# Performance work log

Hardware: AMD Instinct MI355X
Metric: run time of the kernel (lower is better)

Reference implementation:

```python
import jax, jax.numpy as jnp
import numpy as np

# Body-part joint index groups (NTU-25 layout), as in the torch module
TORSO = np.array([0, 1, 2, 3, 20])
LEFT_HAND = np.array([8, 9, 10, 11, 23, 24])
LEFT_LEG = np.array([16, 17, 18, 19])
RIGHT_HAND = np.array([4, 5, 6, 7, 21, 22])
RIGHT_LEG = np.array([12, 13, 14, 15])
GROUPS = [TORSO, LEFT_HAND, LEFT_LEG, RIGHT_HAND, RIGHT_LEG]

N, C, T, V = 64, 256, 64, 25
HID = C // 16


def setup_inputs() -> dict:
    key = jax.random.key(0)
    k = jax.random.split(key, 5)
    x = jax.random.normal(k[0], (N, C, T, V), dtype=jnp.float32)
    # 5 branch MLPs (1x1 convs == linear over channels), stacked on leading axis f
    W1s = jax.random.normal(k[1], (5, HID, C), dtype=jnp.float32) * (1.0 / np.sqrt(C))
    b1s = jax.random.normal(k[2], (5, HID), dtype=jnp.float32) * 0.01
    W2s = jax.random.normal(k[3], (5, C, HID), dtype=jnp.float32) * (1.0 / np.sqrt(HID))
    b2s = jax.random.normal(k[4], (5, C), dtype=jnp.float32) * 0.01
    return {"x": x, "W1s": W1s, "b1s": b1s, "W2s": W2s, "b2s": b2s}


def _branch_mlp(p, W1s, b1s, W2s, b2s):
    # p: [N, C] pooled features; apply all 5 branch MLPs at once -> [N, 5, C]
    h = jax.nn.relu(jnp.einsum("nc,fhc->nfh", p, W1s) + b1s[None])  # [N,5,HID]
    return jnp.einsum("nfh,fch->nfc", h, W2s) + b2s[None]  # [N,5,C]


def reference(x, W1s, b1s, W2s, b2s):
    torso = x[:, :, :, TORSO]  # [N,C,T,5]
    avg = jnp.mean(torso, axis=(2, 3))  # [N,C] (AdaptiveAvgPool2d(1))
    mx = jnp.max(torso, axis=(2, 3))  # [N,C] (AdaptiveMaxPool2d(1))
    gates = jax.nn.sigmoid(_branch_mlp(avg, W1s, b1s, W2s, b2s)
                           + _branch_mlp(mx, W1s, b1s, W2s, b2s))  # [N,5,C]
    parts = [x[:, :, :, idx] * gates[:, i][:, :, None, None]
             for i, idx in enumerate(GROUPS)]
    return jnp.concatenate(parts, axis=3)  # [N,C,T,25]
```

## Files before the change

### kernel.cpp

```cpp
#include <hip/hip_runtime.h>
#include <math.h>

#define NB   64
#define CC   256
#define TT   64
#define VV   25
#define HID  16
#define NG   5
#define ROWF 1600
#define ROWF4 400
#define PAIRS 4

#define TORSO_MASK 0x10000Fu

__constant__ int PERM_LUT[25] = {
    0|(0<<8), 1|(0<<8), 2|(0<<8), 3|(0<<8), 20|(0<<8),
    8|(1<<8), 9|(1<<8), 10|(1<<8), 11|(1<<8), 23|(1<<8), 24|(1<<8),
    16|(2<<8), 17|(2<<8), 18|(2<<8), 19|(2<<8),
    4|(3<<8), 5|(3<<8), 6|(3<<8), 7|(3<<8), 21|(3<<8), 22|(3<<8),
    12|(4<<8), 13|(4<<8), 14|(4<<8), 15|(4<<8)
};

__global__ void pool_kernel(const float4* __restrict__ x4,
                            float* __restrict__ avg_out,
                            float* __restrict__ max_out) {
    const int wave = threadIdx.x >> 6;
    const int lane = threadIdx.x & 63;
    const int pair = blockIdx.x * 4 + wave;
    const int base4 = pair * ROWF4;

    float s = 0.0f;
    float m = -3.4e38f;
    for (int i = lane; i < ROWF4; i += 64) {
        float4 v = x4[base4 + i];
        const int e = 4 * i;
        int j = e % 25;
        float vals[4] = {v.x, v.y, v.z, v.w};
        #pragma unroll
        for (int k = 0; k < 4; ++k) {
            int jj = j + k;
            if (jj >= 25) jj -= 25;
            if ((TORSO_MASK >> jj) & 1u) {
                s += vals[k];
                m = fmaxf(m, vals[k]);
            }
        }
    }
    #pragma unroll
    for (int off = 32; off >= 1; off >>= 1) {
        s += __shfl_xor(s, off, 64);
        m = fmaxf(m, __shfl_xor(m, off, 64));
    }
    if (lane == 0) {
        avg_out[pair] = s * (1.0f / (TT * 5));
        max_out[pair] = m;
    }
}

__global__ void gates_kernel(const float* __restrict__ avg_in,
                             const float* __restrict__ max_in,
                             const float* __restrict__ W1s,
                             const float* __restrict__ b1s,
                             const float* __restrict__ W2s,
                             const float* __restrict__ b2s,
                             float* __restrict__ gates) {
    __shared__ float4 sAvg[CC / 4];
    __shared__ float4 sMax[CC / 4];
    __shared__ float sHA[NG * HID];
    __shared__ float sHM[NG * HID];

    const int n = blockIdx.x;
    const int tid = threadIdx.x;

    if (tid < 64)       sAvg[tid]      = reinterpret_cast<const float4*>(avg_in + n * CC)[tid];
    else if (tid < 128) sMax[tid - 64] = reinterpret_cast<const float4*>(max_in + n * CC)[tid - 64];
    __syncthreads();

    if (tid < 2 * NG * HID) {
        const int type = tid / (NG * HID);
        const int rem  = tid % (NG * HID);
        const float4* p = type ? sMax : sAvg;
        const float4* w = reinterpret_cast<const float4*>(W1s + rem * CC);
        float h = b1s[rem];
        #pragma unroll 8
        for (int c4 = 0; c4 < CC / 4; ++c4) {
            float4 a = w[c4], b = p[c4];
            h += a.x * b.x + a.y * b.y + a.z * b.z + a.w * b.w;
        }
        h = fmaxf(h, 0.0f);
        if (type) sHM[rem] = h; else sHA[rem] = h;
    }
    __syncthreads();

    const int c = tid;
    #pragma unroll
    for (int f = 0; f < NG; ++f) {
        const float4* w2 = reinterpret_cast<const float4*>(W2s + (f * CC + c) * HID);
        float g = 2.0f * b2s[f * CC + c];
        #pragma unroll
        for (int j4 = 0; j4 < HID / 4; ++j4) {
            float4 w = w2[j4];
            const int jb = f * HID + j4 * 4;
            g += w.x * (sHA[jb + 0] + sHM[jb + 0]);
            g += w.y * (sHA[jb + 1] + sHM[jb + 1]);
            g += w.z * (sHA[jb + 2] + sHM[jb + 2]);
            g += w.w * (sHA[jb + 3] + sHM[jb + 3]);
        }
        gates[(n * NG + f) * CC + c] = 1.0f / (1.0f + expf(-g));
    }
}

__global__ void apply_kernel(const float4* __restrict__ x4,
                             const float* __restrict__ gates,
                             float4* __restrict__ out4) {
    __shared__ float lds[PAIRS * ROWF];
    __shared__ float sg[PAIRS * NG];
    __shared__ int sLut[VV];

    const int tid = threadIdx.x;
    const int nc0 = blockIdx.x * PAIRS;
    const int base4 = nc0 * ROWF4;

    #pragma unroll
    for (int i = tid; i < PAIRS * ROWF4; i += 256) {
        reinterpret_cast<float4*>(lds)[i] = x4[base4 + i];
    }
    if (tid < PAIRS * NG) {
        const int q = tid / NG, f = tid % NG;
        const int nc = nc0 + q;
        sg[tid] = gates[((nc >> 8) * NG + f) * CC + (nc & (CC - 1))];
    }
    if (tid < VV) sLut[tid] = PERM_LUT[tid];
    __syncthreads();

    #pragma unroll
    for (int i = tid; i < PAIRS * ROWF4; i += 256) {
        const int q = i / ROWF4;
        const int e0 = 4 * (i - q * ROWF4);
        int row = e0 / 25;
        int p   = e0 - row * 25;
        const float* lrow = lds + q * ROWF;
        const float* gq   = sg + q * NG;
        float r[4];
        #pragma unroll
        for (int k = 0; k < 4; ++k) {
            const int lut = sLut[p];
            r[k] = lrow[row * 25 + (lut & 0xFF)] * gq[lut >> 8];
            ++p;
            if (p >= 25) { p = 0; ++row; }
        }
        out4[base4 + i] = make_float4(r[0], r[1], r[2], r[3]);
    }
}

extern "C" void kernel_launch(void* const* d_in, const int* in_sizes, int n_in,
                              void* d_out, int out_size, void* d_ws, size_t ws_size,
                              hipStream_t stream) {
    const float* x   = (const float*)d_in[0];
    const float* W1s = (const float*)d_in[1];
    const float* b1s = (const float*)d_in[2];
    const float* W2s = (const float*)d_in[3];
    const float* b2s = (const float*)d_in[4];

    float* avg   = (float*)d_ws;
    float* mx    = avg + NB * CC;
    float* gates = mx + NB * CC;

    pool_kernel<<<(NB * CC) / 4, 256, 0, stream>>>(
        (const float4*)x, avg, mx);

    gates_kernel<<<NB, CC, 0, stream>>>(avg, mx, W1s, b1s, W2s, b2s, gates);

    apply_kernel<<<(NB * CC) / PAIRS, 256, 0, stream>>>(
        (const float4*)x, gates, (float4*)d_out);
}
```

Baseline: 219.5 us.

## Fuse pool, gate MLP and apply into one cooperative persistent kernel

Replaces the three-kernel pipeline with a single cooperative kernel of 1024 blocks. Each block pools its 16 (n,c) rows, then a grid-wide sync follows, and each block recomputes the hidden MLP layer for its batch item and builds gates for its own channels. It then gathers and scales its rows in chunks through LDS. This removes two kernel launches and the global gates round-trip, and it aims to reuse its own pooled rows from cache. In exchange it adds a grid barrier, redundant W1 work in every block, and a dependence on all 1024 blocks being co-resident, with the old path kept as a fallback.

```diff
diff --git a/kernel.cpp b/kernel.cpp
--- a/kernel.cpp
+++ b/kernel.cpp
@@ -1,5 +1,8 @@
 #include <hip/hip_runtime.h>
+#include <hip/hip_cooperative_groups.h>
 #include <math.h>
+
+namespace cg = cooperative_groups;
 
 #define NB   64
 #define CC   256
@@ -9,17 +12,147 @@
 #define NG   5
 #define ROWF 1600
 #define ROWF4 400
+
+#define TORSO_MASK 0x10000Fu
+
+#define GRID   1024
+#define BPB    16
+#define CHUNK  4
+#define NCHUNK (BPB / CHUNK)
+
 #define PAIRS 4
 
-#define TORSO_MASK 0x10000Fu
-
-__constant__ int PERM_LUT[25] = {
+__constant__ int PERM_LUT[VV] = {
     0|(0<<8), 1|(0<<8), 2|(0<<8), 3|(0<<8), 20|(0<<8),
     8|(1<<8), 9|(1<<8), 10|(1<<8), 11|(1<<8), 23|(1<<8), 24|(1<<8),
     16|(2<<8), 17|(2<<8), 18|(2<<8), 19|(2<<8),
     4|(3<<8), 5|(3<<8), 6|(3<<8), 7|(3<<8), 21|(3<<8), 22|(3<<8),
     12|(4<<8), 13|(4<<8), 14|(4<<8), 15|(4<<8)
 };
+
+__global__ __launch_bounds__(256, 4)
+void fused_kernel(const float4* __restrict__ x4,
+                  const float* __restrict__ W1s,
+                  const float* __restrict__ b1s,
+                  const float* __restrict__ W2s,
+                  const float* __restrict__ b2s,
+                  float* __restrict__ avg_g,
+                  float* __restrict__ max_g,
+                  float4* __restrict__ out4)
+{
+    __shared__ float  lds[CHUNK * ROWF];
+    __shared__ float4 sAvg[CC / 4];
+    __shared__ float4 sMax[CC / 4];
+    __shared__ float  sHA[NG * HID];
+    __shared__ float  sHM[NG * HID];
+    __shared__ float  sg[BPB * NG];
+    __shared__ int    sLut[VV];
+
+    const int tid  = threadIdx.x;
+    const int wave = tid >> 6;
+    const int lane = tid & 63;
+    const int nc0  = blockIdx.x * BPB;
+
+    const unsigned long long M2 = (unsigned long long)TORSO_MASK
+                                | ((unsigned long long)TORSO_MASK << 25);
+    #pragma unroll
+    for (int p = 0; p < BPB / 4; ++p) {
+        const int pair  = nc0 + wave * (BPB / 4) + p;
+        const int base4 = pair * ROWF4;
+        float s = 0.0f;
+        float m = -3.4e38f;
+        for (int i = lane; i < ROWF4; i += 64) {
+            float4 v = x4[base4 + i];
+            const int e = 4 * i;
+            const int j = e % 25;
+            const unsigned bits = (unsigned)((M2 >> j) & 0xFULL);
+            if (bits & 1u) { s += v.x; m = fmaxf(m, v.x); }
+            if (bits & 2u) { s += v.y; m = fmaxf(m, v.y); }
+            if (bits & 4u) { s += v.z; m = fmaxf(m, v.z); }
+            if (bits & 8u) { s += v.w; m = fmaxf(m, v.w); }
+        }
+        #pragma unroll
+        for (int off = 32; off >= 1; off >>= 1) {
+            s += __shfl_xor(s, off, 64);
+            m = fmaxf(m, __shfl_xor(m, off, 64));
+        }
+        if (lane == 0) {
+            avg_g[pair] = s * (1.0f / (TT * 5));
+            max_g[pair] = m;
+        }
+    }
+
+    __threadfence();
+    cg::this_grid().sync();
+
+    const int n  = nc0 >> 8;
+    const int c0 = nc0 & (CC - 1);
+
+    if (tid < 64)       sAvg[tid]      = reinterpret_cast<const float4*>(avg_g + n * CC)[tid];
+    else if (tid < 128) sMax[tid - 64] = reinterpret_cast<const float4*>(max_g + n * CC)[tid - 64];
+    if (tid < VV) sLut[tid] = PERM_LUT[tid];
+    __syncthreads();
+
+    if (tid < 2 * NG * HID) {
+        const int type = tid / (NG * HID);
+        const int rem  = tid % (NG * HID);
+        const float4* pv = type ? sMax : sAvg;
+        const float4* w  = reinterpret_cast<const float4*>(W1s + rem * CC);
+        float h = b1s[rem];
+        #pragma unroll 8
+        for (int c4 = 0; c4 < CC / 4; ++c4) {
+            float4 a = w[c4], b = pv[c4];
+            h += a.x * b.x + a.y * b.y + a.z * b.z + a.w * b.w;
+        }
+        h = fmaxf(h, 0.0f);
+        if (type) sHM[rem] = h; else sHA[rem] = h;
+    }
+    __syncthreads();
+
+    if (tid < BPB * NG) {
+        const int q = tid / NG;
+        const int f = tid % NG;
+        const int c = c0 + q;
+        const float4* w2 = reinterpret_cast<const float4*>(W2s + (f * CC + c) * HID);
+        float g = 2.0f * b2s[f * CC + c];
+        #pragma unroll
+        for (int j4 = 0; j4 < HID / 4; ++j4) {
+            float4 w = w2[j4];
+            const int jb = f * HID + 4 * j4;
+            g += w.x * (sHA[jb + 0] + sHM[jb + 0]);
+            g += w.y * (sHA[jb + 1] + sHM[jb + 1]);
+            g += w.z * (sHA[jb + 2] + sHM[jb + 2]);
+            g += w.w * (sHA[jb + 3] + sHM[jb + 3]);
+        }
+        sg[tid] = 1.0f / (1.0f + expf(-g));
+    }
+    __syncthreads();
+
+    for (int ch = 0; ch < NCHUNK; ++ch) {
+        const int base4 = (nc0 + ch * CHUNK) * ROWF4;
+        for (int i = tid; i < CHUNK * ROWF4; i += 256)
+            reinterpret_cast<float4*>(lds)[i] = x4[base4 + i];
+        __syncthreads();
+        for (int i = tid; i < CHUNK * ROWF4; i += 256) {
+            const int q  = i / ROWF4;
+            const int e0 = 4 * (i - q * ROWF4);
+            int row = e0 / 25;
+            int p   = e0 - row * 25;
+            const float* lrow = lds + q * ROWF;
+            const float* gq   = sg + (ch * CHUNK + q) * NG;
+            float r[4];
+            #pragma unroll
+            for (int k = 0; k < 4; ++k) {
+                const int lut = sLut[p];
+                r[k] = lrow[row * 25 + (lut & 0xFF)] * gq[lut >> 8];
+                ++p;
+                if (p >= 25) { p = 0; ++row; }
+            }
+            out4[base4 + i] = make_float4(r[0], r[1], r[2], r[3]);
+        }
+        __syncthreads();
+    }
+}
 
 __global__ void pool_kernel(const float4* __restrict__ x4,
                             float* __restrict__ avg_out,
@@ -156,21 +289,28 @@
 extern "C" void kernel_launch(void* const* d_in, const int* in_sizes, int n_in,
                               void* d_out, int out_size, void* d_ws, size_t ws_size,
                               hipStream_t stream) {
-    const float* x   = (const float*)d_in[0];
-    const float* W1s = (const float*)d_in[1];
-    const float* b1s = (const float*)d_in[2];
-    const float* W2s = (const float*)d_in[3];
-    const float* b2s = (const float*)d_in[4];
+    const float4* x4  = (const float4*)d_in[0];
+    const float*  W1s = (const float*)d_in[1];
+    const float*  b1s = (const float*)d_in[2];
+    const float*  W2s = (const float*)d_in[3];
+    const float*  b2s = (const float*)d_in[4];
 
     float* avg   = (float*)d_ws;
     float* mx    = avg + NB * CC;
     float* gates = mx + NB * CC;
-
-    pool_kernel<<<(NB * CC) / 4, 256, 0, stream>>>(
-        (const float4*)x, avg, mx);
-
-    gates_kernel<<<NB, CC, 0, stream>>>(avg, mx, W1s, b1s, W2s, b2s, gates);
-
-    apply_kernel<<<(NB * CC) / PAIRS, 256, 0, stream>>>(
-        (const float4*)x, gates, (float4*)d_out);
-}
+    float4* o4   = (float4*)d_out;
+
+    void* args[] = { (void*)&x4, (void*)&W1s, (void*)&b1s, (void*)&W2s,
+                     (void*)&b2s, (void*)&avg, (void*)&mx, (void*)&o4 };
+
+    hipError_t err = hipLaunchCooperativeKernel(
+        reinterpret_cast<void*>(fused_kernel),
+        dim3(GRID), dim3(256), args, 0, stream);
+
+    if (err != hipSuccess) {
+        (void)hipGetLastError();
+        pool_kernel<<<(NB * CC) / 4, 256, 0, stream>>>(x4, avg, mx);
+        gates_kernel<<<NB, CC, 0, stream>>>(avg, mx, W1s, b1s, W2s, b2s, gates);
+        apply_kernel<<<(NB * CC) / PAIRS, 256, 0, stream>>>(x4, gates, o4);
+    }
+}
```

After: 396.2 us. 80.5% more time.

## Fuse gate MLP into apply kernel and simplify torso mask in pooling

Applied to the files above, without the earlier changes.

Removes the separate gates kernel. Each apply block now recomputes the hidden layer for its sample from the pooled features and computes only the gates for its four channels directly into shared memory. This removes one launch and the gates round trip through global memory, but every block redundantly reads W1s and performs the 256-wide dot products before applying. The pooling kernel also replaces the per-element modulo mask test with a precomputed shifted 64-bit mask lookup.

```diff
diff --git a/kernel.cpp b/kernel.cpp
--- a/kernel.cpp
+++ b/kernel.cpp
@@ -13,7 +13,7 @@
 
 #define TORSO_MASK 0x10000Fu
 
-__constant__ int PERM_LUT[25] = {
+__constant__ int PERM_LUT[VV] = {
     0|(0<<8), 1|(0<<8), 2|(0<<8), 3|(0<<8), 20|(0<<8),
     8|(1<<8), 9|(1<<8), 10|(1<<8), 11|(1<<8), 23|(1<<8), 24|(1<<8),
     16|(2<<8), 17|(2<<8), 18|(2<<8), 19|(2<<8),
@@ -29,22 +29,18 @@
     const int pair = blockIdx.x * 4 + wave;
     const int base4 = pair * ROWF4;
 
+    const unsigned long long M2 = (unsigned long long)TORSO_MASK
+                                | ((unsigned long long)TORSO_MASK << 25);
     float s = 0.0f;
     float m = -3.4e38f;
     for (int i = lane; i < ROWF4; i += 64) {
         float4 v = x4[base4 + i];
-        const int e = 4 * i;
-        int j = e % 25;
-        float vals[4] = {v.x, v.y, v.z, v.w};
-        #pragma unroll
-        for (int k = 0; k < 4; ++k) {
-            int jj = j + k;
-            if (jj >= 25) jj -= 25;
-            if ((TORSO_MASK >> jj) & 1u) {
-                s += vals[k];
-                m = fmaxf(m, vals[k]);
-            }
-        }
+        const int j = (4 * i) % 25;
+        const unsigned bits = (unsigned)((M2 >> j) & 0xFULL);
+        if (bits & 1u) { s += v.x; m = fmaxf(m, v.x); }
+        if (bits & 2u) { s += v.y; m = fmaxf(m, v.y); }
+        if (bits & 4u) { s += v.z; m = fmaxf(m, v.z); }
+        if (bits & 8u) { s += v.w; m = fmaxf(m, v.w); }
     }
     #pragma unroll
     for (int off = 32; off >= 1; off >>= 1) {
@@ -57,34 +53,47 @@
     }
 }
 
-__global__ void gates_kernel(const float* __restrict__ avg_in,
-                             const float* __restrict__ max_in,
-                             const float* __restrict__ W1s,
-                             const float* __restrict__ b1s,
-                             const float* __restrict__ W2s,
-                             const float* __restrict__ b2s,
-                             float* __restrict__ gates) {
+__global__ __launch_bounds__(256)
+void applyg_kernel(const float4* __restrict__ x4,
+                   const float* __restrict__ avg_g,
+                   const float* __restrict__ max_g,
+                   const float* __restrict__ W1s,
+                   const float* __restrict__ b1s,
+                   const float* __restrict__ W2s,
+                   const float* __restrict__ b2s,
+                   float4* __restrict__ out4) {
+    __shared__ float  lds[PAIRS * ROWF];
     __shared__ float4 sAvg[CC / 4];
     __shared__ float4 sMax[CC / 4];
-    __shared__ float sHA[NG * HID];
-    __shared__ float sHM[NG * HID];
+    __shared__ float  sHA[NG * HID];
+    __shared__ float  sHM[NG * HID];
+    __shared__ float  sg[PAIRS * NG];
+    __shared__ int    sLut[VV];
 
-    const int n = blockIdx.x;
-    const int tid = threadIdx.x;
+    const int tid  = threadIdx.x;
+    const int nc0  = blockIdx.x * PAIRS;
+    const int n    = nc0 >> 8;
+    const int c0   = nc0 & (CC - 1);
+    const int base4 = nc0 * ROWF4;
 
-    if (tid < 64)       sAvg[tid]      = reinterpret_cast<const float4*>(avg_in + n * CC)[tid];
-    else if (tid < 128) sMax[tid - 64] = reinterpret_cast<const float4*>(max_in + n * CC)[tid - 64];
+    #pragma unroll
+    for (int i = tid; i < PAIRS * ROWF4; i += 256) {
+        reinterpret_cast<float4*>(lds)[i] = x4[base4 + i];
+    }
+    if (tid < 64)       sAvg[tid]      = reinterpret_cast<const float4*>(avg_g + n * CC)[tid];
+    else if (tid < 128) sMax[tid - 64] = reinterpret_cast<const float4*>(max_g + n * CC)[tid - 64];
+    if (tid < VV) sLut[tid] = PERM_LUT[tid];
     __syncthreads();
 
     if (tid < 2 * NG * HID) {
         const int type = tid / (NG * HID);
         const int rem  = tid % (NG * HID);
-        const float4* p = type ? sMax : sAvg;
-        const float4* w = reinterpret_cast<const float4*>(W1s + rem * CC);
+        const float4* pv = type ? sMax : sAvg;
+        const float4* w  = reinterpret_cast<const float4*>(W1s + rem * CC);
         float h = b1s[rem];
         #pragma unroll 8
         for (int c4 = 0; c4 < CC / 4; ++c4) {
-            float4 a = w[c4], b = p[c4];
+            float4 a = w[c4], b = pv[c4];
             h += a.x * b.x + a.y * b.y + a.z * b.z + a.w * b.w;
         }
         h = fmaxf(h, 0.0f);
@@ -92,50 +101,28 @@
     }
     __syncthreads();
 
-    const int c = tid;
-    #pragma unroll
-    for (int f = 0; f < NG; ++f) {
+    if (tid < PAIRS * NG) {
+        const int q = tid / NG;
+        const int f = tid % NG;
+        const int c = c0 + q;
         const float4* w2 = reinterpret_cast<const float4*>(W2s + (f * CC + c) * HID);
         float g = 2.0f * b2s[f * CC + c];
         #pragma unroll
         for (int j4 = 0; j4 < HID / 4; ++j4) {
             float4 w = w2[j4];
-            const int jb = f * HID + j4 * 4;
+            const int jb = f * HID + 4 * j4;
             g += w.x * (sHA[jb + 0] + sHM[jb + 0]);
             g += w.y * (sHA[jb + 1] + sHM[jb + 1]);
             g += w.z * (sHA[jb + 2] + sHM[jb + 2]);
             g += w.w * (sHA[jb + 3] + sHM[jb + 3]);
         }
-        gates[(n * NG + f) * CC + c] = 1.0f / (1.0f + expf(-g));
+        sg[tid] = 1.0f / (1.0f + expf(-g));
     }
-}
-
-__global__ void apply_kernel(const float4* __restrict__ x4,
-                             const float* __restrict__ gates,
-                             float4* __restrict__ out4) {
-    __shared__ float lds[PAIRS * ROWF];
-    __shared__ float sg[PAIRS * NG];
-    __shared__ int sLut[VV];
-
-    const int tid = threadIdx.x;
-    const int nc0 = blockIdx.x * PAIRS;
-    const int base4 = nc0 * ROWF4;
-
-    #pragma unroll
-    for (int i = tid; i < PAIRS * ROWF4; i += 256) {
-        reinterpret_cast<float4*>(lds)[i] = x4[base4 + i];
-    }
-    if (tid < PAIRS * NG) {
-        const int q = tid / NG, f = tid % NG;
-        const int nc = nc0 + q;
-        sg[tid] = gates[((nc >> 8) * NG + f) * CC + (nc & (CC - 1))];
-    }
-    if (tid < VV) sLut[tid] = PERM_LUT[tid];
     __syncthreads();
 
     #pragma unroll
     for (int i = tid; i < PAIRS * ROWF4; i += 256) {
-        const int q = i / ROWF4;
+        const int q  = i / ROWF4;
         const int e0 = 4 * (i - q * ROWF4);
         int row = e0 / 25;
         int p   = e0 - row * 25;
@@ -156,21 +143,17 @@
 extern "C" void kernel_launch(void* const* d_in, const int* in_sizes, int n_in,
                               void* d_out, int out_size, void* d_ws, size_t ws_size,
                               hipStream_t stream) {
-    const float* x   = (const float*)d_in[0];
-    const float* W1s = (const float*)d_in[1];
-    const float* b1s = (const float*)d_in[2];
-    const float* W2s = (const float*)d_in[3];
-    const float* b2s = (const float*)d_in[4];
+    const float4* x4  = (const float4*)d_in[0];
+    const float*  W1s = (const float*)d_in[1];
+    const float*  b1s = (const float*)d_in[2];
+    const float*  W2s = (const float*)d_in[3];
+    const float*  b2s = (const float*)d_in[4];
 
-    float* avg   = (float*)d_ws;
-    float* mx    = avg + NB * CC;
-    float* gates = mx + NB * CC;
+    float* avg = (float*)d_ws;
+    float* mx  = avg + NB * CC;
 
-    pool_kernel<<<(NB * CC) / 4, 256, 0, stream>>>(
-        (const float4*)x, avg, mx);
+    pool_kernel<<<(NB * CC) / 4, 256, 0, stream>>>(x4, avg, mx);
 
-    gates_kernel<<<NB, CC, 0, stream>>>(avg, mx, W1s, b1s, W2s, b2s, gates);
-
-    apply_kernel<<<(NB * CC) / PAIRS, 256, 0, stream>>>(
-        (const float4*)x, gates, (float4*)d_out);
+    applyg_kernel<<<(NB * CC) / PAIRS, 256, 0, stream>>>(
+        x4, avg, mx, W1s, b1s, W2s, b2s, (float4*)d_out);
 }
```

Measured after the change: 270.6 us. +23.3%, slower.
